# Performance work log

Measured on AMD Instinct MI355X. Metric: run time of the kernel, lower is better.

Reference implementation:

```python
import jax, jax.numpy as jnp
import numpy as np

NEG_SLOPE = 0.2  # PyG GATConv default negative_slope
N_NODES = 50000


def gat_conv(x, src, dst, W, att_src, att_dst, bias, heads, out_ch):
    # x: [N, F_in]; src/dst: [E] (messages flow src -> dst, softmax over dst)
    N = x.shape[0]
    h = (x @ W).reshape(N, heads, out_ch)              # [N,H,C]
    a_src = jnp.sum(h * att_src, axis=-1)              # [N,H]
    a_dst = jnp.sum(h * att_dst, axis=-1)              # [N,H]
    e = jax.nn.leaky_relu(a_src[src] + a_dst[dst], NEG_SLOPE)   # [E,H]
    # numerically stable segment softmax over incoming edges of each dst node
    m = jax.ops.segment_max(e, dst, num_segments=N)    # [N,H]
    e = jnp.exp(e - m[dst])
    denom = jax.ops.segment_sum(e, dst, num_segments=N)
    alpha = e / (denom[dst] + 1e-16)                   # [E,H]
    msg = h[src] * alpha[:, :, None]                   # [E,H,C]
    out = jax.ops.segment_sum(msg, dst, num_segments=N)  # [N,H,C]
    return out.reshape(N, heads * out_ch) + bias


def add_self_loops(edge_index, num_nodes):
    loop = jnp.arange(num_nodes, dtype=edge_index.dtype)
    return jnp.concatenate([edge_index, jnp.stack([loop, loop])], axis=1)


def setup_inputs() -> dict:
    key = jax.random.key(0)
    ks = jax.random.split(key, 10)
    F_in, H, C, F_out = 256, 4, 64, 16
    x = jax.random.normal(ks[0], (N_NODES, F_in), dtype=jnp.float32)
    edge_index = jax.random.randint(ks[1], (2, 800000), 0, N_NODES, dtype=jnp.int64)
    s1 = 1.0 / np.sqrt(F_in)
    s2 = 1.0 / np.sqrt(H * C)
    return {
        "x": x,
        "edge_index": edge_index,
        "W1": jax.random.normal(ks[2], (F_in, H * C), dtype=jnp.float32) * s1,
        "att_src1": jax.random.normal(ks[3], (H, C), dtype=jnp.float32) * s2,
        "att_dst1": jax.random.normal(ks[4], (H, C), dtype=jnp.float32) * s2,
        "b1": jnp.zeros((H * C,), dtype=jnp.float32),
        "W2": jax.random.normal(ks[5], (H * C, F_out), dtype=jnp.float32) * s2,
        "att_src2": jax.random.normal(ks[6], (1, F_out), dtype=jnp.float32) * 0.25,
        "att_dst2": jax.random.normal(ks[7], (1, F_out), dtype=jnp.float32) * 0.25,
        "b2": jnp.zeros((F_out,), dtype=jnp.float32),
    }


def reference(x, edge_index, W1, att_src1, att_dst1, b1, W2, att_src2, att_dst2, b2):
    ei = add_self_loops(edge_index, x.shape[0])
    src, dst = ei[0], ei[1]
    H1, C1 = att_src1.shape
    h = gat_conv(x, src, dst, W1, att_src1, att_dst1, b1, H1, C1)
    h = jax.nn.relu(h)
    # F.dropout(training=False) is identity in eval mode
    H2, C2 = att_src2.shape
    out = gat_conv(h, src, dst, W2, att_src2, att_dst2, b2, H2, C2)
    return jax.nn.log_softmax(out, axis=1)
```

## Files before the change

### kernel.cpp

```cpp
#include <hip/hip_runtime.h>
#include <math.h>


typedef __attribute__((ext_vector_type(8))) short bf16x8;
typedef __attribute__((ext_vector_type(8))) unsigned short u16x8;
typedef __attribute__((ext_vector_type(4))) float f32x4;
typedef __attribute__((ext_vector_type(2))) float f32x2;

#define BCAP 1536

static __device__ inline unsigned short f2bf(float f) {
    unsigned u = __builtin_bit_cast(unsigned, f);
    unsigned r = (u + 0x7FFF + ((u >> 16) & 1)) >> 16;
    return (unsigned short)r;
}
static __device__ inline float bf2f(unsigned short u) {
    unsigned v = ((unsigned)u) << 16;
    return __builtin_bit_cast(float, v);
}
static __device__ inline float lrelu(float x) { return x > 0.f ? x : 0.2f * x; }

__global__ __launch_bounds__(256) void k_prep_w1t(const float* __restrict__ W1,
                                                  short* __restrict__ w1t,
                                                  int* __restrict__ fill_bkt,
                                                  int nbuk) {
    int idx = blockIdx.x * 256 + threadIdx.x;
    if (idx < nbuk) fill_bkt[idx] = 0;
    int n = idx >> 8, k = idx & 255;
    w1t[n * 256 + k] = (short)f2bf(W1[k * 256 + n]);
}

__global__ __launch_bounds__(256) void k_bucketize(const int* __restrict__ ei,
                                                   int* __restrict__ fill_bkt,
                                                   uint2* __restrict__ tmp,
                                                   int E0, int nbuk) {
    __shared__ int hist[1024];
    __shared__ int base[1024];
    const int t = threadIdx.x;
    const int e0 = blockIdx.x * 4096;
    for (int b = t; b < nbuk; b += 256) hist[b] = 0;
    __syncthreads();
    int ss[16], ds[16];
    int nm = 0;
#pragma unroll
    for (int k = 0; k < 16; ++k) {
        int e = e0 + t + k * 256;
        if (e < E0) {
            ss[nm] = ei[e];
            ds[nm] = ei[E0 + e];
            atomicAdd(&hist[ds[nm] >> 6], 1);
            ++nm;
        }
    }
    __syncthreads();
    for (int b = t; b < nbuk; b += 256) {
        int c = hist[b];
        base[b] = c ? atomicAdd(&fill_bkt[b], c) : 0;
        hist[b] = 0;
    }
    __syncthreads();
    for (int k = 0; k < nm; ++k) {
        int b = ds[k] >> 6;
        int r = base[b] + atomicAdd(&hist[b], 1);
        if (r < BCAP) tmp[(long)b * BCAP + r] = make_uint2((unsigned)ss[k], (unsigned)ds[k]);
    }
}

__global__ __launch_bounds__(1024) void k_bucket_scan(const int* __restrict__ fill_bkt,
                                                      int* __restrict__ bbase,
                                                      int* __restrict__ off,
                                                      int N, int nbuk) {
    __shared__ int s[1024];
    int t = threadIdx.x;
    int cnt = 0;
    if (t < nbuk) {
        int nodec = min(64, N - t * 64);
        cnt = min(fill_bkt[t], BCAP) + nodec;
    }
    s[t] = cnt;
    __syncthreads();
    for (int o = 1; o < 1024; o <<= 1) {
        int v = (t >= o) ? s[t - o] : 0;
        __syncthreads();
        s[t] += v;
        __syncthreads();
    }
    if (t < nbuk) bbase[t] = s[t] - cnt;
    if (t == nbuk - 1) { bbase[nbuk] = s[t]; off[N] = s[t]; }
}

__global__ __launch_bounds__(256) void k_csr_fill(const uint2* __restrict__ tmp,
                                                  const int* __restrict__ fill_bkt,
                                                  const int* __restrict__ bbase,
                                                  int* __restrict__ off,
                                                  int* __restrict__ csr, int N) {
    __shared__ int hist[64];
    __shared__ int loff[64];
    __shared__ int lfill[64];
    const int b = blockIdx.x;
    const int t = threadIdx.x;
    if (t < 64) { hist[t] = 0; lfill[t] = 0; }
    __syncthreads();
    int cnt = min(fill_bkt[b], BCAP);
    const uint2* tp = tmp + (long)b * BCAP;
    for (int i = t; i < cnt; i += 256)
        atomicAdd(&hist[tp[i].y & 63], 1);
    __syncthreads();
    if (t < 64) {
        int v = hist[t] + 1;
        int incl = v;
#pragma unroll
        for (int o = 1; o < 64; o <<= 1) {
            int u = __shfl_up(incl, o);
            if (t >= (unsigned)o) incl += u;
        }
        int lo = bbase[b] + incl - v;
        loff[t] = lo;
        int d = b * 64 + t;
        if (d < N) off[d] = lo;
    }
    __syncthreads();
    for (int i = t; i < cnt; i += 256) {
        uint2 e = tp[i];
        int dl = e.y & 63;
        int r = atomicAdd(&lfill[dl], 1);
        csr[loff[dl] + r] = (int)e.x;
    }
    __syncthreads();
    if (t < 64) {
        int d = b * 64 + t;
        if (d < N) csr[loff[t] + hist[t]] = d;
    }
}

__global__ __launch_bounds__(256) void k_gemm1_mfma(const float* __restrict__ A,
                                                    const short* __restrict__ Bt,
                                                    const float* __restrict__ att_s,
                                                    const float* __restrict__ att_d,
                                                    unsigned char* __restrict__ C8,
                                                    float* __restrict__ a1s,
                                                    float* __restrict__ a1d,
                                                    int M) {
    __shared__ short As[128][40];
    __shared__ short Bs[128][40];
    const int bm = blockIdx.y * 128;
    const int bn = blockIdx.x * 128;
    const int tid = threadIdx.x;
    const int lane = tid & 63;
    const int wave = tid >> 6;
    const int wm = (wave >> 1) * 64;
    const int wn = (wave & 1) * 64;
    const int l15 = lane & 15;
    const int l4 = lane >> 4;

    const int sr = tid >> 1;
    const int sh = (tid & 1) * 16;

    f32x4 acc[4][4] = {};

    for (int k0 = 0; k0 < 256; k0 += 32) {
        {
            float v[16];
            if (bm + sr < M) {
                const float* p = &A[(long)(bm + sr) * 256 + k0 + sh];
#pragma unroll
                for (int q = 0; q < 4; ++q) {
                    float4 fv = *(const float4*)(p + q * 4);
                    v[q * 4 + 0] = fv.x; v[q * 4 + 1] = fv.y;
                    v[q * 4 + 2] = fv.z; v[q * 4 + 3] = fv.w;
                }
            } else {
#pragma unroll
                for (int q = 0; q < 16; ++q) v[q] = 0.f;
            }
            short b[16];
#pragma unroll
            for (int q = 0; q < 16; ++q) b[q] = (short)f2bf(v[q]);
            *(bf16x8*)&As[sr][sh] = *(bf16x8*)&b[0];
            *(bf16x8*)&As[sr][sh + 8] = *(bf16x8*)&b[8];
        }
        {
            const short* p = &Bt[(long)(bn + sr) * 256 + k0 + sh];
            bf16x8 b0 = *(const bf16x8*)p;
            bf16x8 b1 = *(const bf16x8*)(p + 8);
            *(bf16x8*)&Bs[sr][sh] = b0;
            *(bf16x8*)&Bs[sr][sh + 8] = b1;
        }
        __syncthreads();

        bf16x8 af[4], bfr[4];
#pragma unroll
        for (int i = 0; i < 4; ++i)
            af[i] = *(const bf16x8*)&As[wm + i * 16 + l15][l4 * 8];
#pragma unroll
        for (int j = 0; j < 4; ++j)
            bfr[j] = *(const bf16x8*)&Bs[wn + j * 16 + l15][l4 * 8];
#pragma unroll
        for (int i = 0; i < 4; ++i)
#pragma unroll
            for (int j = 0; j < 4; ++j)
                acc[i][j] = __builtin_amdgcn_mfma_f32_16x16x32_bf16(af[i], bfr[j], acc[i][j], 0, 0, 0);
        __syncthreads();
    }

    const int h = (bn + wn) >> 6;
    float aws[4], awd[4];
#pragma unroll
    for (int j = 0; j < 4; ++j) {
        aws[j] = att_s[h * 64 + j * 16 + l15];
        awd[j] = att_d[h * 64 + j * 16 + l15];
    }

#pragma unroll
    for (int i = 0; i < 4; ++i) {
#pragma unroll
        for (int r = 0; r < 4; ++r) {
            float sv = 0.f, dv = 0.f;
#pragma unroll
            for (int j = 0; j < 4; ++j) {
                sv += acc[i][j][r] * aws[j];
                dv += acc[i][j][r] * awd[j];
            }
#pragma unroll
            for (int o = 1; o < 16; o <<= 1) {
                sv += __shfl_xor(sv, o);
                dv += __shfl_xor(dv, o);
            }
            int row = bm + wm + i * 16 + l4 * 4 + r;
            if (row < M) {
                if (l15 == 0) { a1s[row * 4 + h] = sv; a1d[row * 4 + h] = dv; }
#pragma unroll
                for (int j = 0; j < 4; ++j) {
                    float vv = acc[i][j][r];
                    C8[(long)row * 256 + bn + wn + j * 16 + l15] =
                        (unsigned char)(__builtin_amdgcn_cvt_pk_fp8_f32(vv, vv, 0, false) & 0xFF);
                }
            }
        }
    }
}

__global__ __launch_bounds__(256) void k_expden1(const int* __restrict__ off,
                                                 const int* __restrict__ csr,
                                                 const float* __restrict__ as1,
                                                 const float* __restrict__ ad1,
                                                 float* __restrict__ alphaE,
                                                 float* __restrict__ dinv, int N) {
    int wid = blockIdx.x * 4 + (threadIdx.x >> 6);
    int lane = threadIdx.x & 63;
    if (wid >= N) return;
    int begin = off[wid], end = off[wid + 1];
    int h = lane >> 4, t = lane & 15;
    float adh = ad1[wid * 4 + h];
    float den = 0.f;
    for (int j = begin + t; j < end; j += 16) {
        float ex = __expf(lrelu(as1[csr[j] * 4 + h] + adh));
        alphaE[j * 4 + h] = ex;
        den += ex;
    }
#pragma unroll
    for (int o = 1; o < 16; o <<= 1) den += __shfl_xor(den, o);
    if (t == 0) dinv[wid * 4 + h] = 1.f / (den + 1e-16f);
}

__global__ __launch_bounds__(256) void k_gather1(const unsigned char* __restrict__ h1f8,
                                                 const int* __restrict__ off,
                                                 const int* __restrict__ csr,
                                                 const float* __restrict__ alphaE,
                                                 const float* __restrict__ dinv,
                                                 const float* __restrict__ b1,
                                                 unsigned short* __restrict__ out1b,
                                                 int N) {
    int wid = blockIdx.x * 4 + (threadIdx.x >> 6);
    int lane = threadIdx.x & 63;
    if (wid >= N) return;
    int begin = off[wid], end = off[wid + 1];
    const int es = lane >> 4;
    const int cl = lane & 15;
    f32x2 acc2[8] = {};
#pragma unroll 2
    for (int j0 = begin; j0 < end; j0 += 4) {
        int j = j0 + es;
        bool valid = j < end;
        int jc = valid ? j : begin;
        int s = csr[jc];
        float a = valid ? alphaE[jc * 4 + (cl >> 2)] : 0.f;
        f32x2 av = {a, a};
        uint4 v = *(const uint4*)&h1f8[(long)s * 256 + cl * 16];
        unsigned w[4] = {v.x, v.y, v.z, v.w};
#pragma unroll
        for (int q = 0; q < 4; ++q) {
            f32x2 lo = __builtin_amdgcn_cvt_pk_f32_fp8((int)w[q], false);
            f32x2 hi = __builtin_amdgcn_cvt_pk_f32_fp8((int)w[q], true);
            acc2[q * 2 + 0] += av * lo;
            acc2[q * 2 + 1] += av * hi;
        }
    }
    float accf[16];
#pragma unroll
    for (int q = 0; q < 8; ++q) { accf[2 * q] = acc2[q].x; accf[2 * q + 1] = acc2[q].y; }
#pragma unroll
    for (int q = 0; q < 16; ++q) {
        accf[q] += __shfl_xor(accf[q], 16);
        accf[q] += __shfl_xor(accf[q], 32);
    }
    if (lane < 16) {
        float inv = dinv[wid * 4 + (cl >> 2)];
        unsigned pk[8];
#pragma unroll
        for (int q = 0; q < 8; ++q) {
            float v0 = fmaxf(accf[q * 2 + 0] * inv + b1[cl * 16 + q * 2 + 0], 0.f);
            float v1 = fmaxf(accf[q * 2 + 1] * inv + b1[cl * 16 + q * 2 + 1], 0.f);
            pk[q] = (unsigned)f2bf(v0) | ((unsigned)f2bf(v1) << 16);
        }
        unsigned short* dst = &out1b[(long)wid * 256 + cl * 16];
        *(uint4*)dst = make_uint4(pk[0], pk[1], pk[2], pk[3]);
        *(uint4*)(dst + 8) = make_uint4(pk[4], pk[5], pk[6], pk[7]);
    }
}

__global__ __launch_bounds__(256) void k_gemm2(const unsigned short* __restrict__ Xb,
                                               const float* __restrict__ W,
                                               const float* __restrict__ att_s,
                                               const float* __restrict__ att_d,
                                               float* __restrict__ h2,
                                               float* __restrict__ a2s,
                                               float* __restrict__ a2d, int N) {
    __shared__ float Ws[256 * 16];
    for (int i = threadIdx.x; i < 1024; i += 256)
        ((float4*)Ws)[i] = ((const float4*)W)[i];
    __syncthreads();
    int r = threadIdx.x >> 4, c = threadIdx.x & 15;
    int row = blockIdx.x * 16 + r;
    if (row >= N) return;
    const unsigned short* xr = Xb + (long)row * 256;
    float acc = 0.f;
    for (int k = 0; k < 256; k += 8) {
        u16x8 xv = *(const u16x8*)&xr[k];
#pragma unroll
        for (int q = 0; q < 8; ++q) acc += bf2f(xv[q]) * Ws[(k + q) * 16 + c];
    }
    h2[row * 16 + c] = acc;
    float vs = acc * att_s[c];
    float vd = acc * att_d[c];
    for (int o = 1; o < 16; o <<= 1) { vs += __shfl_xor(vs, o); vd += __shfl_xor(vd, o); }
    if (c == 0) { a2s[row] = vs; a2d[row] = vd; }
}

__global__ __launch_bounds__(256) void k_gather2(const float* __restrict__ h2,
                                                 const int* __restrict__ off,
                                                 const int* __restrict__ csr,
                                                 const float* __restrict__ a2s,
                                                 const float* __restrict__ a2d,
                                                 const float* __restrict__ b2,
                                                 float* __restrict__ out, int N) {
    int wid = blockIdx.x * 4 + (threadIdx.x >> 6);
    int lane = threadIdx.x & 63;
    if (wid >= N) return;
    int begin = off[wid], end = off[wid + 1];
    float adh = a2d[wid];
    float den = 0.f;
    for (int j = begin + lane; j < end; j += 64)
        den += __expf(lrelu(a2s[csr[j]] + adh));
#pragma unroll
    for (int o = 32; o; o >>= 1) den += __shfl_xor(den, o);
    float inv = 1.f / (den + 1e-16f);
    const int es = lane >> 4;
    const int c = lane & 15;
    float acc = 0.f;
#pragma unroll 2
    for (int j0 = begin; j0 < end; j0 += 4) {
        int j = j0 + es;
        bool valid = j < end;
        int jc = valid ? j : begin;
        int s = csr[jc];
        float a = valid ? __expf(lrelu(a2s[s] + adh)) : 0.f;
        acc += a * h2[(long)s * 16 + c];
    }
    acc += __shfl_xor(acc, 16);
    acc += __shfl_xor(acc, 32);
    float v = acc * inv + b2[c];
    float mx = v;
    for (int o = 1; o < 16; o <<= 1) mx = fmaxf(mx, __shfl_xor(mx, o));
    float se = __expf(v - mx);
    for (int o = 1; o < 16; o <<= 1) se += __shfl_xor(se, o);
    float r = v - mx - logf(se);
    if (lane < 16) out[(long)wid * 16 + c] = r;
}

extern "C" void kernel_launch(void* const* d_in, const int* in_sizes, int n_in,
                              void* d_out, int out_size, void* d_ws, size_t ws_size,
                              hipStream_t stream) {
    const float* x    = (const float*)d_in[0];
    const int*   ei   = (const int*)d_in[1];
    const float* W1   = (const float*)d_in[2];
    const float* as1w = (const float*)d_in[3];
    const float* ad1w = (const float*)d_in[4];
    const float* b1   = (const float*)d_in[5];
    const float* W2   = (const float*)d_in[6];
    const float* as2w = (const float*)d_in[7];
    const float* ad2w = (const float*)d_in[8];
    const float* b2   = (const float*)d_in[9];
    float* out = (float*)d_out;

    const int N    = in_sizes[0] / 256;
    const int E0   = in_sizes[1] / 2;
    const int Etot = E0 + N;
    const int NBUK = (N + 63) >> 6;

    char* p = (char*)d_ws;
    unsigned char*  h1f8  = (unsigned char*)p;  p += (size_t)N * 256;
    unsigned short* out1b = (unsigned short*)p; p += (size_t)N * 256 * sizeof(short);
    float* h2     = (float*)p; p += (size_t)N * 16 * sizeof(float);
    float* a1s    = (float*)p; p += (size_t)N * 4 * sizeof(float);
    float* a1d    = (float*)p; p += (size_t)N * 4 * sizeof(float);
    float* a2s    = (float*)p; p += (size_t)N * sizeof(float);
    float* a2d    = (float*)p; p += (size_t)N * sizeof(float);
    float* alphaE = (float*)p; p += (size_t)Etot * 4 * sizeof(float);
    float* dinv   = (float*)p; p += (size_t)N * 4 * sizeof(float);
    int*   off    = (int*)p;   p += (size_t)(N + 1) * sizeof(int);
    int*   bbase  = (int*)p;   p += (size_t)(NBUK + 1) * sizeof(int);
    int*   fillbk = (int*)p;   p += (size_t)NBUK * sizeof(int);
    short* w1t    = (short*)p; p += (size_t)256 * 256 * sizeof(short);
    int*   csr    = (int*)p;   p += (size_t)Etot * sizeof(int);
    uint2* tmp    = (uint2*)p; p += (size_t)NBUK * BCAP * sizeof(uint2);

    const int NW = (N + 3) / 4;

    hipLaunchKernelGGL(k_prep_w1t, dim3(256), dim3(256), 0, stream, W1, w1t, fillbk, NBUK);

    hipLaunchKernelGGL(k_bucketize, dim3((E0 + 4095) / 4096), dim3(256), 0, stream,
                       ei, fillbk, tmp, E0, NBUK);
    hipLaunchKernelGGL(k_bucket_scan, dim3(1), dim3(1024), 0, stream,
                       fillbk, bbase, off, N, NBUK);
    hipLaunchKernelGGL(k_csr_fill, dim3(NBUK), dim3(256), 0, stream,
                       tmp, fillbk, bbase, off, csr, N);

    hipLaunchKernelGGL(k_gemm1_mfma, dim3(2, (N + 127) / 128), dim3(256), 0, stream,
                       x, w1t, as1w, ad1w, h1f8, a1s, a1d, N);
    hipLaunchKernelGGL(k_expden1, dim3(NW), dim3(256), 0, stream,
                       off, csr, a1s, a1d, alphaE, dinv, N);
    hipLaunchKernelGGL(k_gather1, dim3(NW), dim3(256), 0, stream,
                       h1f8, off, csr, alphaE, dinv, b1, out1b, N);

    hipLaunchKernelGGL(k_gemm2, dim3((N + 15) / 16), dim3(256), 0, stream,
                       out1b, W2, as2w, ad2w, h2, a2s, a2d, N);
    hipLaunchKernelGGL(k_gather2, dim3(NW), dim3(256), 0, stream,
                       h2, off, csr, a2s, a2d, b2, out, N);
}
```

Baseline: 264.0 us.

## Fuse bucket scan into CSR fill and exp/denominator into layer-1 gather

Removes the single-block bucket prefix-scan kernel. Each CSR-fill block now computes its own base offset by summing the preceding bucket counts with one wavefront. It also merges the edge-score exp/denominator pass into the layer-1 gather kernel, so each wave computes its own normalizer and drops the dinv buffer and its round trip. This cuts two launches and some global traffic, at the cost of redundant prefix sums across blocks (quadratic in bucket count). The gather now reads alphaE values written by other lanes of the same wave, relying only on a block-level fence.

```diff
diff --git a/kernel.cpp b/kernel.cpp
--- a/kernel.cpp
+++ b/kernel.cpp
@@ -66,37 +66,15 @@
     }
 }
 
-__global__ __launch_bounds__(1024) void k_bucket_scan(const int* __restrict__ fill_bkt,
-                                                      int* __restrict__ bbase,
-                                                      int* __restrict__ off,
-                                                      int N, int nbuk) {
-    __shared__ int s[1024];
-    int t = threadIdx.x;
-    int cnt = 0;
-    if (t < nbuk) {
-        int nodec = min(64, N - t * 64);
-        cnt = min(fill_bkt[t], BCAP) + nodec;
-    }
-    s[t] = cnt;
-    __syncthreads();
-    for (int o = 1; o < 1024; o <<= 1) {
-        int v = (t >= o) ? s[t - o] : 0;
-        __syncthreads();
-        s[t] += v;
-        __syncthreads();
-    }
-    if (t < nbuk) bbase[t] = s[t] - cnt;
-    if (t == nbuk - 1) { bbase[nbuk] = s[t]; off[N] = s[t]; }
-}
-
 __global__ __launch_bounds__(256) void k_csr_fill(const uint2* __restrict__ tmp,
                                                   const int* __restrict__ fill_bkt,
-                                                  const int* __restrict__ bbase,
                                                   int* __restrict__ off,
-                                                  int* __restrict__ csr, int N) {
+                                                  int* __restrict__ csr,
+                                                  int N, int nbuk) {
     __shared__ int hist[64];
     __shared__ int loff[64];
     __shared__ int lfill[64];
+    __shared__ int sbase;
     const int b = blockIdx.x;
     const int t = threadIdx.x;
     if (t < 64) { hist[t] = 0; lfill[t] = 0; }
@@ -105,6 +83,18 @@
     const uint2* tp = tmp + (long)b * BCAP;
     for (int i = t; i < cnt; i += 256)
         atomicAdd(&hist[tp[i].y & 63], 1);
+    if (t >= 64 && t < 128) {
+        int l = t - 64;
+        int acc = 0;
+        for (int i = l; i < b; i += 64) acc += min(fill_bkt[i], BCAP);
+#pragma unroll
+        for (int o = 1; o < 64; o <<= 1) acc += __shfl_xor(acc, o);
+        if (l == 0) sbase = acc + 64 * b;
+        if (b == nbuk - 1 && l == 0) {
+            int tot = acc + 64 * b + min(fill_bkt[b], BCAP) + (N - b * 64);
+            off[N] = tot;
+        }
+    }
     __syncthreads();
     if (t < 64) {
         int v = hist[t] + 1;
@@ -114,7 +104,7 @@
             int u = __shfl_up(incl, o);
             if (t >= (unsigned)o) incl += u;
         }
-        int lo = bbase[b] + incl - v;
+        int lo = sbase + incl - v;
         loff[t] = lo;
         int d = b * 64 + t;
         if (d < N) off[d] = lo;
@@ -240,34 +230,12 @@
     }
 }
 
-__global__ __launch_bounds__(256) void k_expden1(const int* __restrict__ off,
+__global__ __launch_bounds__(256) void k_gather1(const unsigned char* __restrict__ h1f8,
+                                                 const int* __restrict__ off,
                                                  const int* __restrict__ csr,
                                                  const float* __restrict__ as1,
                                                  const float* __restrict__ ad1,
                                                  float* __restrict__ alphaE,
-                                                 float* __restrict__ dinv, int N) {
-    int wid = blockIdx.x * 4 + (threadIdx.x >> 6);
-    int lane = threadIdx.x & 63;
-    if (wid >= N) return;
-    int begin = off[wid], end = off[wid + 1];
-    int h = lane >> 4, t = lane & 15;
-    float adh = ad1[wid * 4 + h];
-    float den = 0.f;
-    for (int j = begin + t; j < end; j += 16) {
-        float ex = __expf(lrelu(as1[csr[j] * 4 + h] + adh));
-        alphaE[j * 4 + h] = ex;
-        den += ex;
-    }
-#pragma unroll
-    for (int o = 1; o < 16; o <<= 1) den += __shfl_xor(den, o);
-    if (t == 0) dinv[wid * 4 + h] = 1.f / (den + 1e-16f);
-}
-
-__global__ __launch_bounds__(256) void k_gather1(const unsigned char* __restrict__ h1f8,
-                                                 const int* __restrict__ off,
-                                                 const int* __restrict__ csr,
-                                                 const float* __restrict__ alphaE,
-                                                 const float* __restrict__ dinv,
                                                  const float* __restrict__ b1,
                                                  unsigned short* __restrict__ out1b,
                                                  int N) {
@@ -275,8 +243,28 @@
     int lane = threadIdx.x & 63;
     if (wid >= N) return;
     int begin = off[wid], end = off[wid + 1];
+
+    float inv;
+    {
+        int h = lane >> 4, t = lane & 15;
+        float adh = ad1[wid * 4 + h];
+        float den = 0.f;
+        for (int j = begin + t; j < end; j += 16) {
+            float ex = __expf(lrelu(as1[csr[j] * 4 + h] + adh));
+            alphaE[j * 4 + h] = ex;
+            den += ex;
+        }
+#pragma unroll
+        for (int o = 1; o < 16; o <<= 1) den += __shfl_xor(den, o);
+        inv = 1.f / (den + 1e-16f);
+    }
+    __threadfence_block();
+
     const int es = lane >> 4;
     const int cl = lane & 15;
+    const int hc = cl >> 2;
+    const float inv_c = __shfl(inv, hc * 16);
+
     f32x2 acc2[8] = {};
 #pragma unroll 2
     for (int j0 = begin; j0 < end; j0 += 4) {
@@ -284,7 +272,7 @@
         bool valid = j < end;
         int jc = valid ? j : begin;
         int s = csr[jc];
-        float a = valid ? alphaE[jc * 4 + (cl >> 2)] : 0.f;
+        float a = valid ? alphaE[jc * 4 + hc] : 0.f;
         f32x2 av = {a, a};
         uint4 v = *(const uint4*)&h1f8[(long)s * 256 + cl * 16];
         unsigned w[4] = {v.x, v.y, v.z, v.w};
@@ -305,12 +293,11 @@
         accf[q] += __shfl_xor(accf[q], 32);
     }
     if (lane < 16) {
-        float inv = dinv[wid * 4 + (cl >> 2)];
         unsigned pk[8];
 #pragma unroll
         for (int q = 0; q < 8; ++q) {
-            float v0 = fmaxf(accf[q * 2 + 0] * inv + b1[cl * 16 + q * 2 + 0], 0.f);
-            float v1 = fmaxf(accf[q * 2 + 1] * inv + b1[cl * 16 + q * 2 + 1], 0.f);
+            float v0 = fmaxf(accf[q * 2 + 0] * inv_c + b1[cl * 16 + q * 2 + 0], 0.f);
+            float v1 = fmaxf(accf[q * 2 + 1] * inv_c + b1[cl * 16 + q * 2 + 1], 0.f);
             pk[q] = (unsigned)f2bf(v0) | ((unsigned)f2bf(v1) << 16);
         }
         unsigned short* dst = &out1b[(long)wid * 256 + cl * 16];
@@ -417,9 +404,7 @@
     float* a2s    = (float*)p; p += (size_t)N * sizeof(float);
     float* a2d    = (float*)p; p += (size_t)N * sizeof(float);
     float* alphaE = (float*)p; p += (size_t)Etot * 4 * sizeof(float);
-    float* dinv   = (float*)p; p += (size_t)N * 4 * sizeof(float);
     int*   off    = (int*)p;   p += (size_t)(N + 1) * sizeof(int);
-    int*   bbase  = (int*)p;   p += (size_t)(NBUK + 1) * sizeof(int);
     int*   fillbk = (int*)p;   p += (size_t)NBUK * sizeof(int);
     short* w1t    = (short*)p; p += (size_t)256 * 256 * sizeof(short);
     int*   csr    = (int*)p;   p += (size_t)Etot * sizeof(int);
@@ -431,17 +416,13 @@
 
     hipLaunchKernelGGL(k_bucketize, dim3((E0 + 4095) / 4096), dim3(256), 0, stream,
                        ei, fillbk, tmp, E0, NBUK);
-    hipLaunchKernelGGL(k_bucket_scan, dim3(1), dim3(1024), 0, stream,
-                       fillbk, bbase, off, N, NBUK);
     hipLaunchKernelGGL(k_csr_fill, dim3(NBUK), dim3(256), 0, stream,
-                       tmp, fillbk, bbase, off, csr, N);
+                       tmp, fillbk, off, csr, N, NBUK);
 
     hipLaunchKernelGGL(k_gemm1_mfma, dim3(2, (N + 127) / 128), dim3(256), 0, stream,
                        x, w1t, as1w, ad1w, h1f8, a1s, a1d, N);
-    hipLaunchKernelGGL(k_expden1, dim3(NW), dim3(256), 0, stream,
-                       off, csr, a1s, a1d, alphaE, dinv, N);
     hipLaunchKernelGGL(k_gather1, dim3(NW), dim3(256), 0, stream,
-                       h1f8, off, csr, alphaE, dinv, b1, out1b, N);
+                       h1f8, off, csr, a1s, a1d, alphaE, b1, out1b, N);
 
     hipLaunchKernelGGL(k_gemm2, dim3((N + 15) / 16), dim3(256), 0, stream,
                        out1b, W2, as2w, ad2w, h2, a2s, a2d, N);
```

New measurement: 257.6 us. -2.4%, faster.
